# Kernel optimization log

Measured on AMD Instinct MI355X. Metric: run time of the kernel, lower is better.

## Reference

```python
import jax, jax.numpy as jnp
import numpy as np

B, N, DIN, HID, DOUT = 1024, 128, 256, 256, 256
KDIM = 4 * N  # fcq/fck output dim = n_node * 4


def setup_inputs() -> dict:
    key = jax.random.key(0)
    ks = jax.random.split(key, 11)
    s = 0.05
    x = jax.random.normal(ks[0], (B, N, DIN), dtype=jnp.float32)
    # binary attention mask in {0,1}
    mask = jax.random.randint(ks[1], (B, N, N), 0, 2).astype(jnp.float32)
    Wv = jax.random.normal(ks[2], (DIN, HID), dtype=jnp.float32) * s
    bv = jax.random.normal(ks[3], (HID,), dtype=jnp.float32) * s
    Wq = jax.random.normal(ks[4], (DIN, KDIM), dtype=jnp.float32) * s
    bq = jax.random.normal(ks[5], (KDIM,), dtype=jnp.float32) * s
    Wk = jax.random.normal(ks[6], (DIN, KDIM), dtype=jnp.float32) * s
    bk = jax.random.normal(ks[7], (KDIM,), dtype=jnp.float32) * s
    Wo = jax.random.normal(ks[8], (HID, DOUT), dtype=jnp.float32) * s
    bo = jax.random.normal(ks[9], (DOUT,), dtype=jnp.float32) * s
    return {"x": x, "mask": mask, "Wv": Wv, "bv": bv, "Wq": Wq, "bq": bq,
            "Wk": Wk, "bk": bk, "Wo": Wo, "bo": bo}


def reference(x, mask, Wv, bv, Wq, bq, Wk, bk, Wo, bo):
    # v: [B,N,HID], q/k: [B,N,4N]
    v = jax.nn.relu(jnp.einsum('bnd,dh->bnh', x, Wv) + bv)
    q = jax.nn.relu(jnp.einsum('bnd,dk->bnk', x, Wq) + bq)
    k = jax.nn.relu(jnp.einsum('bnd,dk->bnk', x, Wk) + bk)
    # scores: bmm(q, k^T) -> [B,N,N]
    scores = jnp.einsum('bnk,bmk->bnm', q, k)
    val = scores * mask - 1000.0 * (1.0 - mask)
    att = jax.nn.softmax(val, axis=2)
    ctx = jnp.einsum('bnm,bmh->bnh', att, v)  # [B,N,HID]
    out = jax.nn.relu(jnp.einsum('bnh,hd->bnd', ctx, Wo) + bo)
    return out, att
```

## Files before the change

### kernel.cpp

```cpp
#include <hip/hip_runtime.h>
#include <cstdint>
#include <cstddef>

#define B_SZ 1024
#define N_SZ 128
#define DIN 256
#define HID 256
#define DOUT 256
#define KD 512

typedef unsigned short u16;
typedef _Float16 f16x8 __attribute__((ext_vector_type(8)));
typedef float floatx4 __attribute__((ext_vector_type(4)));
typedef unsigned short u16x8 __attribute__((ext_vector_type(8)));
typedef unsigned short u16x4 __attribute__((ext_vector_type(4)));

#define MFMA16(a,b,c) __builtin_amdgcn_mfma_f32_16x16x32_f16(a, b, c, 0, 0, 0)

__device__ __forceinline__ u16 f2h(float f) {
    _Float16 h = (_Float16)f;
    return *(u16*)&h;
}

__device__ __forceinline__ void barx() {
    asm volatile("" ::: "memory");
    __builtin_amdgcn_s_barrier();
    asm volatile("" ::: "memory");
}
__device__ __forceinline__ void bar_lgkm() {
    asm volatile("s_waitcnt lgkmcnt(0)" ::: "memory");
    __builtin_amdgcn_s_barrier();
    asm volatile("" ::: "memory");
}

#define XS_OFF  0
#define QS_OFF  65536
#define KS_OFF  81920
#define ATT_OFF 65536
#define WD_OFF  98304
#define RED_OFF 98304

__global__ __launch_bounds__(512, 2)
void fused_att(const float* __restrict__ x,   const float* __restrict__ mask,
               const u16* __restrict__ Wq_t,  const float* __restrict__ bq,
               const u16* __restrict__ Wk_t,  const float* __restrict__ bk,
               const u16* __restrict__ Wv_t,  const float* __restrict__ bv,
               const u16* __restrict__ Wo_t,  const float* __restrict__ bo,
               float* __restrict__ out,       float* __restrict__ att)
{
    __shared__ char LD[131072];

    const int tid  = threadIdx.x;
    const int wid  = tid >> 6;
    const int lane = tid & 63;
    const int l16  = lane & 15;
    const int quad = lane >> 4;
    const int b    = blockIdx.x;

    const int swm = (wid >> 2) * 64;
    const int swn = (wid & 3) * 32;
    const int qm0 = (wid >> 1) * 32;
    const int qn0 = (wid & 1) * 32;

    const int srow  = tid >> 3;
    const int sg    = tid & 7;
    const int swz16 = (sg * 16) ^ ((srow & 7) << 4);

    auto waddr = [&](const u16* Wb, int ch) -> const u16x8* {
        int kdv = ch >> 2, kcv = ch & 3;
        return (const u16x8*)(Wb + ((size_t)(kdv * 64) + srow) * DIN + kcv * 64 + sg * 8);
    };
    auto stage_writeQK = [&](int buf, u16x8 q8, u16x8 k8) {
        char* base = LD + WD_OFF + buf * 16384 + srow * 128 + swz16;
        *(u16x8*)base          = q8;
        *(u16x8*)(base + 8192) = k8;
    };
    auto load256 = [&](const u16* Wb, int kc, u16x8* r4) {
#pragma unroll
        for (int p = 0; p < 4; ++p)
            r4[p] = *(const u16x8*)(Wb + (size_t)(p * 64 + srow) * DIN + kc * 64 + sg * 8);
    };
    auto stage_write256 = [&](const u16x8* r4) {
#pragma unroll
        for (int p = 0; p < 4; ++p)
            *(u16x8*)(LD + WD_OFF + (p * 64 + srow) * 128 + swz16) = r4[p];
    };

    u16x8 rq[2], rk[2];
    rq[0] = *waddr(Wq_t, 0); rk[0] = *waddr(Wk_t, 0);
    rq[1] = *waddr(Wq_t, 1); rk[1] = *waddr(Wk_t, 1);

    {
        const float* xb = x + (size_t)b * (N_SZ * DIN);
        int row = tid >> 2;
        int c0  = (tid & 3) * 64;
        int sw  = (row & 7) << 4;
        const float* xr = xb + (size_t)row * DIN;
#pragma unroll
        for (int u = 0; u < 8; ++u) {
            int col = c0 + u * 8;
            float4 f0 = *(const float4*)(xr + col);
            float4 f1 = *(const float4*)(xr + col + 4);
            u16x8 o;
            o[0] = f2h(f0.x); o[1] = f2h(f0.y); o[2] = f2h(f0.z); o[3] = f2h(f0.w);
            o[4] = f2h(f1.x); o[5] = f2h(f1.y); o[6] = f2h(f1.z); o[7] = f2h(f1.w);
            *(u16x8*)(LD + ((row * 512 + col * 2) ^ sw)) = o;
        }
    }
    stage_writeQK(0, rq[0], rk[0]);
    bar_lgkm();

    f16x8 xa[2][8];
#pragma unroll
    for (int i = 0; i < 2; ++i)
#pragma unroll
        for (int t = 0; t < 8; ++t) {
            int r = qm0 + i * 16 + l16;
            int kofs = t * 32 + quad * 8;
            xa[i][t] = *(const f16x8*)(LD + ((r * 512 + kofs * 2) ^ ((r & 7) << 4)));
        }

    floatx4 sacc[4][2];
#pragma unroll
    for (int i = 0; i < 4; i++)
#pragma unroll
        for (int j = 0; j < 2; j++) sacc[i][j] = floatx4{0.f, 0.f, 0.f, 0.f};

#pragma unroll 1
    for (int kd = 0; kd < 8; ++kd) {
        float bqv[2], bkv[2];
#pragma unroll
        for (int j = 0; j < 2; j++) {
            int col = kd * 64 + qn0 + j * 16 + l16;
            bqv[j] = bq[col];
            bkv[j] = bk[col];
        }
        floatx4 qa[2][2], ka[2][2];
#pragma unroll
        for (int i = 0; i < 2; i++)
#pragma unroll
            for (int j = 0; j < 2; j++) {
                qa[i][j] = floatx4{0.f, 0.f, 0.f, 0.f};
                ka[i][j] = floatx4{0.f, 0.f, 0.f, 0.f};
            }

#pragma unroll
        for (int kc = 0; kc < 4; ++kc) {
            const int ch  = kd * 4 + kc;
            const int par = kc & 1;
            if (ch + 2 < 32) {
                rq[par] = *waddr(Wq_t, ch + 2);
                rk[par] = *waddr(Wk_t, ch + 2);
            }
            const char* WQ = LD + WD_OFF + par * 16384;
            const char* WK = WQ + 8192;
            __builtin_amdgcn_s_setprio(1);
#pragma unroll
            for (int ks = 0; ks < 2; ++ks) {
                f16x8 qf[2], kf[2];
#pragma unroll
                for (int j = 0; j < 2; ++j) {
                    int n  = qn0 + j * 16 + l16;
                    int by = (n * 128) + (((ks * 32 + quad * 8) * 2) ^ ((n & 7) << 4));
                    qf[j] = *(const f16x8*)(WQ + by);
                    kf[j] = *(const f16x8*)(WK + by);
                }
#pragma unroll
                for (int i = 0; i < 2; i++)
#pragma unroll
                    for (int j = 0; j < 2; j++) {
                        qa[i][j] = MFMA16(xa[i][kc * 2 + ks], qf[j], qa[i][j]);
                        ka[i][j] = MFMA16(xa[i][kc * 2 + ks], kf[j], ka[i][j]);
                    }
            }
            __builtin_amdgcn_s_setprio(0);
            if (ch + 1 < 32) stage_writeQK(par ^ 1, rq[par ^ 1], rk[par ^ 1]);
            bar_lgkm();
        }

#pragma unroll
        for (int i = 0; i < 2; i++)
#pragma unroll
            for (int j = 0; j < 2; j++)
#pragma unroll
                for (int r = 0; r < 4; r++) {
                    int rw_ = qm0 + i * 16 + quad * 4 + r;
                    int cl  = qn0 + j * 16 + l16;
                    int by  = (rw_ * 128) + ((cl * 2) ^ ((rw_ & 7) << 4));
                    *(u16*)(LD + QS_OFF + by) = f2h(fmaxf(qa[i][j][r] + bqv[j], 0.f));
                    *(u16*)(LD + KS_OFF + by) = f2h(fmaxf(ka[i][j][r] + bkv[j], 0.f));
                }
        bar_lgkm();

        __builtin_amdgcn_s_setprio(1);
#pragma unroll
        for (int ks = 0; ks < 2; ++ks) {
            f16x8 saf[4], sbf[2];
            int kb2 = (ks * 32 + quad * 8) * 2;
#pragma unroll
            for (int i = 0; i < 4; i++) {
                int r = swm + i * 16 + l16;
                saf[i] = *(const f16x8*)(LD + QS_OFF + (r * 128) + (kb2 ^ ((r & 7) << 4)));
            }
#pragma unroll
            for (int j = 0; j < 2; j++) {
                int n = swn + j * 16 + l16;
                sbf[j] = *(const f16x8*)(LD + KS_OFF + (n * 128) + (kb2 ^ ((n & 7) << 4)));
            }
#pragma unroll
            for (int i = 0; i < 4; i++)
#pragma unroll
                for (int j = 0; j < 2; j++)
                    sacc[i][j] = MFMA16(saf[i], sbf[j], sacc[i][j]);
        }
        __builtin_amdgcn_s_setprio(0);
    }

    u16x8 rw[4];
    load256(Wv_t, 0, rw);
    {
        const float* mb = mask + (size_t)b * (N_SZ * N_SZ);
        float mreg[4][4][2];
#pragma unroll
        for (int i = 0; i < 4; i++)
#pragma unroll
            for (int r = 0; r < 4; r++) {
                int row = swm + i * 16 + quad * 4 + r;
#pragma unroll
                for (int j = 0; j < 2; j++)
                    mreg[i][r][j] = mb[row * N_SZ + swn + j * 16 + l16];
            }

        float* REDm = (float*)(LD + RED_OFF);
        float* REDs = REDm + 512;
        float rmax[4][4];
#pragma unroll
        for (int i = 0; i < 4; i++) {
#pragma unroll
            for (int r = 0; r < 4; r++) {
                float mx = -1e30f;
#pragma unroll
                for (int j = 0; j < 2; j++) {
                    float mval = mreg[i][r][j];
                    float val  = sacc[i][j][r] * mval - 1000.f * (1.f - mval);
                    sacc[i][j][r] = val;
                    mx = fmaxf(mx, val);
                }
#pragma unroll
                for (int s = 1; s < 16; s <<= 1) mx = fmaxf(mx, __shfl_xor(mx, s, 64));
                rmax[i][r] = mx;
            }
        }
        if (l16 == 0) {
#pragma unroll
            for (int i = 0; i < 4; i++)
#pragma unroll
                for (int r = 0; r < 4; r++)
                    REDm[(wid & 3) * 128 + swm + i * 16 + quad * 4 + r] = rmax[i][r];
        }
        bar_lgkm();
#pragma unroll
        for (int i = 0; i < 4; i++)
#pragma unroll
            for (int r = 0; r < 4; r++) {
                int row = swm + i * 16 + quad * 4 + r;
                rmax[i][r] = fmaxf(fmaxf(REDm[row], REDm[128 + row]),
                                   fmaxf(REDm[256 + row], REDm[384 + row]));
            }

        float rsum[4][4];
#pragma unroll
        for (int i = 0; i < 4; i++) {
#pragma unroll
            for (int r = 0; r < 4; r++) {
                float s = 0.f;
#pragma unroll
                for (int j = 0; j < 2; j++) {
                    float e = __expf(sacc[i][j][r] - rmax[i][r]);
                    sacc[i][j][r] = e;
                    s += e;
                }
#pragma unroll
                for (int t = 1; t < 16; t <<= 1) s += __shfl_xor(s, t, 64);
                rsum[i][r] = s;
            }
        }
        if (l16 == 0) {
#pragma unroll
            for (int i = 0; i < 4; i++)
#pragma unroll
                for (int r = 0; r < 4; r++)
                    REDs[(wid & 3) * 128 + swm + i * 16 + quad * 4 + r] = rsum[i][r];
        }
        bar_lgkm();

        float* ao = att + (size_t)b * (N_SZ * N_SZ);
#pragma unroll
        for (int i = 0; i < 4; i++) {
#pragma unroll
            for (int r = 0; r < 4; r++) {
                int row = swm + i * 16 + quad * 4 + r;
                float inv = 1.f / (REDs[row] + REDs[128 + row] +
                                   REDs[256 + row] + REDs[384 + row]);
#pragma unroll
                for (int j = 0; j < 2; j++) {
                    int col = swn + j * 16 + l16;
                    float a = sacc[i][j][r] * inv;
                    ao[row * N_SZ + col] = a;
                    int by = (row * 256) + ((col * 2) ^ ((row & 7) << 4));
                    *(u16*)(LD + ATT_OFF + by) = f2h(a);
                }
            }
        }
        bar_lgkm();
    }

    floatx4 ctxa[4][4];
#pragma unroll
    for (int i = 0; i < 4; i++)
#pragma unroll
        for (int j = 0; j < 4; j++) ctxa[i][j] = floatx4{0.f, 0.f, 0.f, 0.f};

    {
        floatx4 va[4][4];
#pragma unroll
        for (int i = 0; i < 4; i++)
#pragma unroll
            for (int j = 0; j < 4; j++) va[i][j] = floatx4{0.f, 0.f, 0.f, 0.f};

#pragma unroll
        for (int kc = 0; kc < 4; ++kc) {
            stage_write256(rw);
            if (kc < 3) load256(Wv_t, kc + 1, rw);
            else        load256(Wo_t, 0, rw);
            bar_lgkm();
            __builtin_amdgcn_s_setprio(1);
#pragma unroll
            for (int ks = 0; ks < 2; ++ks) {
                int kofs = kc * 64 + ks * 32 + quad * 8;
                f16x8 af[4], wf[4];
#pragma unroll
                for (int i = 0; i < 4; i++) {
                    int r = swm + i * 16 + l16;
                    af[i] = *(const f16x8*)(LD + ((r * 512 + kofs * 2) ^ ((r & 7) << 4)));
                }
#pragma unroll
                for (int jj = 0; jj < 4; jj++) {
                    int n = (jj >> 1) * 128 + swn + (jj & 1) * 16 + l16;
                    wf[jj] = *(const f16x8*)(LD + WD_OFF + (n * 128) +
                                             (((ks * 32 + quad * 8) * 2) ^ ((n & 7) << 4)));
                }
#pragma unroll
                for (int i = 0; i < 4; i++)
#pragma unroll
                    for (int jj = 0; jj < 4; jj++)
                        va[i][jj] = MFMA16(af[i], wf[jj], va[i][jj]);
            }
            __builtin_amdgcn_s_setprio(0);
            barx();
        }

        float bvv[4];
#pragma unroll
        for (int jj = 0; jj < 4; jj++)
            bvv[jj] = bv[(jj >> 1) * 128 + swn + (jj & 1) * 16 + l16];
#pragma unroll
        for (int i = 0; i < 4; i++)
#pragma unroll
            for (int jj = 0; jj < 4; jj++) {
                int m0 = swm + i * 16 + quad * 4;
                int h  = (jj >> 1) * 128 + swn + (jj & 1) * 16 + l16;
                u16x4 pk;
#pragma unroll
                for (int r = 0; r < 4; r++)
                    pk[r] = f2h(fmaxf(va[i][jj][r] + bvv[jj], 0.f));
                int by = (h * 256) + ((m0 * 2) ^ ((h & 7) << 4));
                *(u16x4*)(LD + by) = pk;
            }
        bar_lgkm();

        __builtin_amdgcn_s_setprio(1);
#pragma unroll
        for (int ks = 0; ks < 4; ++ks) {
            int kb2 = (ks * 32 + quad * 8) * 2;
            f16x8 paf[4], pbf[4];
#pragma unroll
            for (int i = 0; i < 4; i++) {
                int r = swm + i * 16 + l16;
                paf[i] = *(const f16x8*)(LD + ATT_OFF + (r * 256) + (kb2 ^ ((r & 7) << 4)));
            }
#pragma unroll
            for (int jj = 0; jj < 4; jj++) {
                int h = (jj >> 1) * 128 + swn + (jj & 1) * 16 + l16;
                pbf[jj] = *(const f16x8*)(LD + (h * 256) + (kb2 ^ ((h & 7) << 4)));
            }
#pragma unroll
            for (int i = 0; i < 4; i++)
#pragma unroll
                for (int jj = 0; jj < 4; jj++)
                    ctxa[i][jj] = MFMA16(paf[i], pbf[jj], ctxa[i][jj]);
        }
        __builtin_amdgcn_s_setprio(0);
        barx();
    }

#pragma unroll
    for (int i = 0; i < 4; i++)
#pragma unroll
        for (int jj = 0; jj < 4; jj++)
#pragma unroll
            for (int r = 0; r < 4; r++) {
                int row = swm + i * 16 + quad * 4 + r;
                int col = (jj >> 1) * 128 + swn + (jj & 1) * 16 + l16;
                int by  = (row * 512) + ((col * 2) ^ ((row & 7) << 4));
                *(u16*)(LD + by) = f2h(ctxa[i][jj][r]);
            }
    bar_lgkm();

    {
        floatx4 oa[4][4];
#pragma unroll
        for (int i = 0; i < 4; i++)
#pragma unroll
            for (int j = 0; j < 4; j++) oa[i][j] = floatx4{0.f, 0.f, 0.f, 0.f};

#pragma unroll
        for (int kc = 0; kc < 4; ++kc) {
            stage_write256(rw);
            if (kc < 3) load256(Wo_t, kc + 1, rw);
            bar_lgkm();
            __builtin_amdgcn_s_setprio(1);
#pragma unroll
            for (int ks = 0; ks < 2; ++ks) {
                int kofs = kc * 64 + ks * 32 + quad * 8;
                f16x8 caf[4], wof[4];
#pragma unroll
                for (int i = 0; i < 4; i++) {
                    int r = swm + i * 16 + l16;
                    caf[i] = *(const f16x8*)(LD + ((r * 512 + kofs * 2) ^ ((r & 7) << 4)));
                }
#pragma unroll
                for (int jj = 0; jj < 4; jj++) {
                    int n = (jj >> 1) * 128 + swn + (jj & 1) * 16 + l16;
                    wof[jj] = *(const f16x8*)(LD + WD_OFF + (n * 128) +
                                              (((ks * 32 + quad * 8) * 2) ^ ((n & 7) << 4)));
                }
#pragma unroll
                for (int i = 0; i < 4; i++)
#pragma unroll
                    for (int jj = 0; jj < 4; jj++)
                        oa[i][jj] = MFMA16(caf[i], wof[jj], oa[i][jj]);
            }
            __builtin_amdgcn_s_setprio(0);
            if (kc < 3) barx();
        }

        float* ob = out + (size_t)b * (N_SZ * DOUT);
        float bov[4];
#pragma unroll
        for (int jj = 0; jj < 4; jj++)
            bov[jj] = bo[(jj >> 1) * 128 + swn + (jj & 1) * 16 + l16];
#pragma unroll
        for (int i = 0; i < 4; i++)
#pragma unroll
            for (int jj = 0; jj < 4; jj++)
#pragma unroll
                for (int r = 0; r < 4; r++) {
                    int row = swm + i * 16 + quad * 4 + r;
                    int col = (jj >> 1) * 128 + swn + (jj & 1) * 16 + l16;
                    ob[(size_t)row * DOUT + col] = fmaxf(oa[i][jj][r] + bov[jj], 0.f);
                }
    }
}

#define SQK (DIN * KD)
#define SVO (DIN * HID)
__global__ __launch_bounds__(256)
void wtrans_all(const float* __restrict__ Wq, const float* __restrict__ Wk,
                const float* __restrict__ Wv, const float* __restrict__ Wo,
                u16* __restrict__ Wq_t, u16* __restrict__ Wk_t,
                u16* __restrict__ Wv_t, u16* __restrict__ Wo_t)
{
    int idx = blockIdx.x * 256 + threadIdx.x;
    if (idx < SQK) {
        int k = idx / KD, n = idx % KD;
        Wq_t[(size_t)n * DIN + k] = f2h(Wq[idx]);
    } else if (idx < 2 * SQK) {
        int i = idx - SQK;
        int k = i / KD, n = i % KD;
        Wk_t[(size_t)n * DIN + k] = f2h(Wk[i]);
    } else if (idx < 2 * SQK + SVO) {
        int i = idx - 2 * SQK;
        int k = i / HID, n = i % HID;
        Wv_t[(size_t)n * DIN + k] = f2h(Wv[i]);
    } else if (idx < 2 * SQK + 2 * SVO) {
        int i = idx - 2 * SQK - SVO;
        int k = i / DOUT, n = i % DOUT;
        Wo_t[(size_t)n * HID + k] = f2h(Wo[i]);
    }
}

extern "C" void kernel_launch(void* const* d_in, const int* in_sizes, int n_in,
                              void* d_out, int out_size, void* d_ws, size_t ws_size,
                              hipStream_t stream)
{
    const float* x    = (const float*)d_in[0];
    const float* mask = (const float*)d_in[1];
    const float* Wv   = (const float*)d_in[2];
    const float* bv   = (const float*)d_in[3];
    const float* Wq   = (const float*)d_in[4];
    const float* bq   = (const float*)d_in[5];
    const float* Wk   = (const float*)d_in[6];
    const float* bk   = (const float*)d_in[7];
    const float* Wo   = (const float*)d_in[8];
    const float* bo   = (const float*)d_in[9];

    float* out = (float*)d_out;
    float* att = out + (size_t)B_SZ * N_SZ * DOUT;

    char* ws = (char*)d_ws;
    u16* Wq_t = (u16*)ws;
    u16* Wk_t = Wq_t + (size_t)KD * DIN;
    u16* Wv_t = Wk_t + (size_t)KD * DIN;
    u16* Wo_t = Wv_t + (size_t)HID * DIN;

    wtrans_all<<<(2 * SQK + 2 * SVO + 255) / 256, 256, 0, stream>>>(
        Wq, Wk, Wv, Wo, Wq_t, Wk_t, Wv_t, Wo_t);

    fused_att<<<B_SZ, 512, 0, stream>>>(x, mask,
                                        Wq_t, bq, Wk_t, bk, Wv_t, bv, Wo_t, bo,
                                        out, att);

    (void)in_sizes; (void)n_in; (void)out_size; (void)ws_size;
}
```

Before: 469.0 us.

## Read weight MFMA fragments directly from global memory instead of LDS staging

Removes the double-buffered LDS staging of Wq/Wk/Wv/Wo tiles and instead loads the f16 weight fragments for each MFMA straight from global memory (L2/L1 cached). This drops the weight-staging barriers and LDS writes, and shrinks shared memory from 128 KB to 100 KB. The cost is exposed global-load latency inside the MFMA loops with no software prefetch, and redundant per-wave reads of the same weights. A barrier is added at the end of each kd iteration to keep the Q/K tile reuse safe.

Measured after the change: 680.3 us. 1.45x slower.

```diff
diff --git a/kernel.cpp b/kernel.cpp
--- a/kernel.cpp
+++ b/kernel.cpp
@@ -37,7 +37,6 @@
 #define QS_OFF  65536
 #define KS_OFF  81920
 #define ATT_OFF 65536
-#define WD_OFF  98304
 #define RED_OFF 98304
 
 __global__ __launch_bounds__(512, 2)
@@ -48,7 +47,7 @@
                const u16* __restrict__ Wo_t,  const float* __restrict__ bo,
                float* __restrict__ out,       float* __restrict__ att)
 {
-    __shared__ char LD[131072];
+    __shared__ char LD[102400];
 
     const int tid  = threadIdx.x;
     const int wid  = tid >> 6;
@@ -61,34 +60,6 @@
     const int swn = (wid & 3) * 32;
     const int qm0 = (wid >> 1) * 32;
     const int qn0 = (wid & 1) * 32;
-
-    const int srow  = tid >> 3;
-    const int sg    = tid & 7;
-    const int swz16 = (sg * 16) ^ ((srow & 7) << 4);
-
-    auto waddr = [&](const u16* Wb, int ch) -> const u16x8* {
-        int kdv = ch >> 2, kcv = ch & 3;
-        return (const u16x8*)(Wb + ((size_t)(kdv * 64) + srow) * DIN + kcv * 64 + sg * 8);
-    };
-    auto stage_writeQK = [&](int buf, u16x8 q8, u16x8 k8) {
-        char* base = LD + WD_OFF + buf * 16384 + srow * 128 + swz16;
-        *(u16x8*)base          = q8;
-        *(u16x8*)(base + 8192) = k8;
-    };
-    auto load256 = [&](const u16* Wb, int kc, u16x8* r4) {
-#pragma unroll
-        for (int p = 0; p < 4; ++p)
-            r4[p] = *(const u16x8*)(Wb + (size_t)(p * 64 + srow) * DIN + kc * 64 + sg * 8);
-    };
-    auto stage_write256 = [&](const u16x8* r4) {
-#pragma unroll
-        for (int p = 0; p < 4; ++p)
-            *(u16x8*)(LD + WD_OFF + (p * 64 + srow) * 128 + swz16) = r4[p];
-    };
-
-    u16x8 rq[2], rk[2];
-    rq[0] = *waddr(Wq_t, 0); rk[0] = *waddr(Wk_t, 0);
-    rq[1] = *waddr(Wq_t, 1); rk[1] = *waddr(Wk_t, 1);
 
     {
         const float* xb = x + (size_t)b * (N_SZ * DIN);
@@ -107,7 +78,6 @@
             *(u16x8*)(LD + ((row * 512 + col * 2) ^ sw)) = o;
         }
     }
-    stage_writeQK(0, rq[0], rk[0]);
     bar_lgkm();
 
     f16x8 xa[2][8];
@@ -144,26 +114,21 @@
                 ka[i][j] = floatx4{0.f, 0.f, 0.f, 0.f};
             }
 
+        const u16* Wqb = Wq_t + (size_t)(kd * 64) * DIN;
+        const u16* Wkb = Wk_t + (size_t)(kd * 64) * DIN;
+
+        __builtin_amdgcn_s_setprio(1);
 #pragma unroll
         for (int kc = 0; kc < 4; ++kc) {
-            const int ch  = kd * 4 + kc;
-            const int par = kc & 1;
-            if (ch + 2 < 32) {
-                rq[par] = *waddr(Wq_t, ch + 2);
-                rk[par] = *waddr(Wk_t, ch + 2);
-            }
-            const char* WQ = LD + WD_OFF + par * 16384;
-            const char* WK = WQ + 8192;
-            __builtin_amdgcn_s_setprio(1);
 #pragma unroll
             for (int ks = 0; ks < 2; ++ks) {
+                int kofs = kc * 64 + ks * 32 + quad * 8;
                 f16x8 qf[2], kf[2];
 #pragma unroll
                 for (int j = 0; j < 2; ++j) {
-                    int n  = qn0 + j * 16 + l16;
-                    int by = (n * 128) + (((ks * 32 + quad * 8) * 2) ^ ((n & 7) << 4));
-                    qf[j] = *(const f16x8*)(WQ + by);
-                    kf[j] = *(const f16x8*)(WK + by);
+                    size_t off = (size_t)(qn0 + j * 16 + l16) * DIN + kofs;
+                    qf[j] = *(const f16x8*)(Wqb + off);
+                    kf[j] = *(const f16x8*)(Wkb + off);
                 }
 #pragma unroll
                 for (int i = 0; i < 2; i++)
@@ -173,10 +138,8 @@
                         ka[i][j] = MFMA16(xa[i][kc * 2 + ks], kf[j], ka[i][j]);
                     }
             }
-            __builtin_amdgcn_s_setprio(0);
-            if (ch + 1 < 32) stage_writeQK(par ^ 1, rq[par ^ 1], rk[par ^ 1]);
-            bar_lgkm();
-        }
+        }
+        __builtin_amdgcn_s_setprio(0);
 
 #pragma unroll
         for (int i = 0; i < 2; i++)
@@ -214,10 +177,9 @@
                     sacc[i][j] = MFMA16(saf[i], sbf[j], sacc[i][j]);
         }
         __builtin_amdgcn_s_setprio(0);
-    }
-
-    u16x8 rw[4];
-    load256(Wv_t, 0, rw);
+        barx();
+    }
+
     {
         const float* mb = mask + (size_t)b * (N_SZ * N_SZ);
         float mreg[4][4][2];
@@ -328,13 +290,9 @@
 #pragma unroll
             for (int j = 0; j < 4; j++) va[i][j] = floatx4{0.f, 0.f, 0.f, 0.f};
 
+        __builtin_amdgcn_s_setprio(1);
 #pragma unroll
         for (int kc = 0; kc < 4; ++kc) {
-            stage_write256(rw);
-            if (kc < 3) load256(Wv_t, kc + 1, rw);
-            else        load256(Wo_t, 0, rw);
-            bar_lgkm();
-            __builtin_amdgcn_s_setprio(1);
 #pragma unroll
             for (int ks = 0; ks < 2; ++ks) {
                 int kofs = kc * 64 + ks * 32 + quad * 8;
@@ -347,8 +305,7 @@
 #pragma unroll
                 for (int jj = 0; jj < 4; jj++) {
                     int n = (jj >> 1) * 128 + swn + (jj & 1) * 16 + l16;
-                    wf[jj] = *(const f16x8*)(LD + WD_OFF + (n * 128) +
-                                             (((ks * 32 + quad * 8) * 2) ^ ((n & 7) << 4)));
+                    wf[jj] = *(const f16x8*)(Wv_t + (size_t)n * DIN + kofs);
                 }
 #pragma unroll
                 for (int i = 0; i < 4; i++)
@@ -356,9 +313,9 @@
                     for (int jj = 0; jj < 4; jj++)
                         va[i][jj] = MFMA16(af[i], wf[jj], va[i][jj]);
             }
-            __builtin_amdgcn_s_setprio(0);
-            barx();
-        }
+        }
+        __builtin_amdgcn_s_setprio(0);
+        barx();
 
         float bvv[4];
 #pragma unroll
@@ -424,12 +381,9 @@
 #pragma unroll
             for (int j = 0; j < 4; j++) oa[i][j] = floatx4{0.f, 0.f, 0.f, 0.f};
 
+        __builtin_amdgcn_s_setprio(1);
 #pragma unroll
         for (int kc = 0; kc < 4; ++kc) {
-            stage_write256(rw);
-            if (kc < 3) load256(Wo_t, kc + 1, rw);
-            bar_lgkm();
-            __builtin_amdgcn_s_setprio(1);
 #pragma unroll
             for (int ks = 0; ks < 2; ++ks) {
                 int kofs = kc * 64 + ks * 32 + quad * 8;
@@ -442,8 +396,7 @@
 #pragma unroll
                 for (int jj = 0; jj < 4; jj++) {
                     int n = (jj >> 1) * 128 + swn + (jj & 1) * 16 + l16;
-                    wof[jj] = *(const f16x8*)(LD + WD_OFF + (n * 128) +
-                                              (((ks * 32 + quad * 8) * 2) ^ ((n & 7) << 4)));
+                    wof[jj] = *(const f16x8*)(Wo_t + (size_t)n * HID + kofs);
                 }
 #pragma unroll
                 for (int i = 0; i < 4; i++)
@@ -451,9 +404,8 @@
                     for (int jj = 0; jj < 4; jj++)
                         oa[i][jj] = MFMA16(caf[i], wof[jj], oa[i][jj]);
             }
-            __builtin_amdgcn_s_setprio(0);
-            if (kc < 3) barx();
-        }
+        }
+        __builtin_amdgcn_s_setprio(0);
 
         float* ob = out + (size_t)b * (N_SZ * DOUT);
         float bov[4];
```
